# Kernel optimization log

Hardware: AMD Instinct MI355X
Metric: run time of the kernel (lower is better)

Reference implementation:

```python
import jax, jax.numpy as jnp
import numpy as np

B, T, C = 4, 2048, 2048
H = 16
D = C // H  # head_dim = 128


def setup_inputs() -> dict:
    key = jax.random.key(0)
    ks = jax.random.split(key, 11)
    s = 0.02
    return {
        "q": jax.random.normal(ks[0], (B, T, C), jnp.float32),
        "k": jax.random.normal(ks[1], (B, T, C), jnp.float32),
        "v": jax.random.normal(ks[2], (B, T, C), jnp.float32),
        "Wq": jax.random.normal(ks[3], (C, C), jnp.float32) * s,
        "bq": jnp.zeros((C,), jnp.float32),
        "Wk": jax.random.normal(ks[4], (C, C), jnp.float32) * s,
        "bk": jnp.zeros((C,), jnp.float32),
        "Wv": jax.random.normal(ks[5], (C, C), jnp.float32) * s,
        "bv": jnp.zeros((C,), jnp.float32),
        "Wo": jax.random.normal(ks[6], (C, C), jnp.float32) * s,
        "bo": jnp.zeros((C,), jnp.float32),
    }


def reference(q, k, v, Wq, bq, Wk, bk, Wv, bv, Wo, bo):
    # torch Linear: y = x @ W.T + b
    def heads(x, W, b):
        y = x @ W.T + b                      # [B,T,C]
        return y.reshape(B, T, H, D).transpose(0, 2, 1, 3)  # [B,H,T,D]

    q_h = heads(q, Wq, bq)
    k_h = heads(k, Wk, bk)
    v_h = heads(v, Wv, bv)

    scale = D ** -0.5
    scores = jnp.einsum('bhqd,bhkd->bhqk', q_h, k_h) * scale  # [B,H,T,T]
    # causal mask (is_causal=True)
    causal = jnp.tril(jnp.ones((T, T), dtype=bool))
    scores = jnp.where(causal, scores, -jnp.inf)
    probs = jax.nn.softmax(scores, axis=-1)
    out = jnp.einsum('bhqk,bhkd->bhqd', probs, v_h)           # [B,H,T,D]
    out = out.transpose(0, 2, 1, 3).reshape(B, T, C)
    return out @ Wo.T + bo
```

## Files before the change

kernel.cpp:

```cpp
#include <hip/hip_runtime.h>
#include <hip/hip_bf16.h>
#include <cmath>


#define DEV __device__ __forceinline__

typedef short short8 __attribute__((ext_vector_type(8)));
typedef float floatx4 __attribute__((ext_vector_type(4)));

#define LDS16(gp, lp)                                                        \
  __builtin_amdgcn_global_load_lds(                                          \
      (const __attribute__((address_space(1))) void*)(gp),                   \
      (__attribute__((address_space(3))) void*)(lp), 16, 0, 0)

DEV unsigned short f2bf(float f) {
  unsigned u = __builtin_bit_cast(unsigned, f);
  u += 0x7fffu + ((u >> 16) & 1u);
  return (unsigned short)(u >> 16);
}

DEV floatx4 mfma16(short8 a, short8 b, floatx4 c) {
  return __builtin_amdgcn_mfma_f32_16x16x32_bf16(a, b, c, 0, 0, 0);
}

struct Cvt7Args {
  const float* in[7];
  unsigned short* out[7];
  int n4[7];
};

__global__ __launch_bounds__(256) void cvt7_kernel(Cvt7Args a) {
  const int s = blockIdx.y;
  const float* __restrict__ in = a.in[s];
  unsigned short* __restrict__ out = a.out[s];
  const int n4 = a.n4[s];
  int stride = gridDim.x * blockDim.x;
  for (int i = blockIdx.x * blockDim.x + threadIdx.x; i < n4; i += stride) {
    float4 v = reinterpret_cast<const float4*>(in)[i];
    ushort4 o;
    o.x = f2bf(v.x); o.y = f2bf(v.y); o.z = f2bf(v.z); o.w = f2bf(v.w);
    reinterpret_cast<ushort4*>(out)[i] = o;
  }
}

DEV void gemm256_core(const unsigned short* __restrict__ aT,
                      const unsigned short* __restrict__ bT,
                      unsigned short* lds, const int K, floatx4 (&acc)[8][4]) {
  const int t = threadIdx.x;
  const int l = t & 63;
  const int w = t >> 6;
  const int wm = w >> 2, wn = w & 3;
  const int lr = l & 15, lg = l >> 4;
  const int NT = K >> 5;

  const int rA0 = t >> 2;
  const int chA0 = (t & 3) ^ ((rA0 >> 1) & 3);
  const int rA1 = (t + 512) >> 2;
  const int chA1 = (t & 3) ^ ((rA1 >> 1) & 3);

  auto stage = [&](int kt, int buf) {
    unsigned short* dst = lds + buf * 16384;
    const unsigned short* ga = aT + kt * 32;
    const unsigned short* gb = bT + kt * 32;
    LDS16(ga + (size_t)rA0 * K + chA0 * 8, dst + t * 8);
    LDS16(ga + (size_t)rA1 * K + chA1 * 8, dst + (t + 512) * 8);
    LDS16(gb + (size_t)rA0 * K + chA0 * 8, dst + 8192 + t * 8);
    LDS16(gb + (size_t)rA1 * K + chA1 * 8, dst + 8192 + (t + 512) * 8);
  };

  stage(0, 0);
  stage(1, 1);
  stage(2, 2);
  asm volatile("s_waitcnt vmcnt(8)" ::: "memory");
  __builtin_amdgcn_s_barrier();
  asm volatile("" ::: "memory");

  for (int tt = 0; tt < NT; ++tt) {
    const unsigned short* lA = lds + (tt & 3) * 16384;
    const unsigned short* lB = lA + 8192;
    if (tt + 3 < NT) stage(tt + 3, (tt + 3) & 3);
    short8 aF[8], bF[4];
#pragma unroll
    for (int ni = 0; ni < 4; ni++) {
      int row = wn * 64 + ni * 16 + lr;
      bF[ni] = *(const short8*)&lB[row * 32 + ((lg ^ ((row >> 1) & 3)) * 8)];
    }
#pragma unroll
    for (int mi = 0; mi < 8; mi++) {
      int row = wm * 128 + mi * 16 + lr;
      aF[mi] = *(const short8*)&lA[row * 32 + ((lg ^ ((row >> 1) & 3)) * 8)];
    }
    __builtin_amdgcn_s_setprio(1);
#pragma unroll
    for (int mi = 0; mi < 8; mi++)
#pragma unroll
      for (int ni = 0; ni < 4; ni++)
        acc[mi][ni] = mfma16(aF[mi], bF[ni], acc[mi][ni]);
    __builtin_amdgcn_s_setprio(0);
    if (tt + 1 < NT) {
      if (tt + 4 <= NT)
        asm volatile("s_waitcnt vmcnt(8)" ::: "memory");
      else if (tt + 3 == NT)
        asm volatile("s_waitcnt vmcnt(4)" ::: "memory");
      else
        asm volatile("s_waitcnt vmcnt(0)" ::: "memory");
      __builtin_amdgcn_s_barrier();
      asm volatile("" ::: "memory");
    }
  }
}

__global__ __launch_bounds__(512, 2) void gemm256_proj3(
    const unsigned short* __restrict__ qb, const unsigned short* __restrict__ kb,
    const unsigned short* __restrict__ vb, const unsigned short* __restrict__ wqb,
    const unsigned short* __restrict__ wkb, const unsigned short* __restrict__ wvb,
    const float* __restrict__ bq, const float* __restrict__ bk,
    const float* __restrict__ bv, unsigned short* __restrict__ Qp,
    unsigned short* __restrict__ Kp, unsigned short* __restrict__ Vt,
    float qscale) {
  constexpr int K = 2048, N = 2048;
  __shared__ unsigned short lds[65536];
  const int seg = blockIdx.x >> 8;
  int inner = blockIdx.x & 255;
  inner = (inner & 7) * 32 + (inner >> 3);
  const int bm = inner >> 3, bn = inner & 7;

  const unsigned short* A = (seg == 0) ? qb : (seg == 1) ? kb : vb;
  const unsigned short* Bw = (seg == 0) ? wqb : (seg == 1) ? wkb : wvb;
  const float* bias = (seg == 0) ? bq : (seg == 1) ? bk : bv;

  floatx4 zero = {0.f, 0.f, 0.f, 0.f};
  floatx4 acc[8][4];
#pragma unroll
  for (int i = 0; i < 8; i++)
#pragma unroll
    for (int j = 0; j < 4; j++) acc[i][j] = zero;

  gemm256_core(A + (size_t)bm * 256 * K, Bw + (size_t)bn * 256 * K, lds, K, acc);

  const int t = threadIdx.x, l = t & 63, w = t >> 6;
  const int wm = w >> 2, wn = w & 3;
  const int lr = l & 15, lg = l >> 4;
  const float oscale = (seg == 0) ? qscale : 1.0f;
#pragma unroll
  for (int ni = 0; ni < 4; ni++) {
    int gc = bn * 256 + wn * 64 + ni * 16 + lr;
    float bvv = bias[gc];
#pragma unroll
    for (int mi = 0; mi < 8; mi++) {
      int gr0 = bm * 256 + wm * 128 + mi * 16 + lg * 4;
      if (seg == 2) {
        int b = gr0 >> 11, tt0 = gr0 & 2047, h = gc >> 7, d = gc & 127;
        ushort4 v4;
        v4.x = f2bf(acc[mi][ni][0] + bvv);
        v4.y = f2bf(acc[mi][ni][1] + bvv);
        v4.z = f2bf(acc[mi][ni][2] + bvv);
        v4.w = f2bf(acc[mi][ni][3] + bvv);
        *(ushort4*)&Vt[((size_t)(b * 16 + h) << 18) + (d << 11) + tt0] = v4;
      } else {
        unsigned short* dst = (seg == 0) ? Qp : Kp;
#pragma unroll
        for (int r = 0; r < 4; r++)
          dst[(size_t)(gr0 + r) * N + gc] =
              f2bf((acc[mi][ni][r] + bvv) * oscale);
      }
    }
  }
}

__global__ __launch_bounds__(512, 2) void gemm256_out(
    const unsigned short* __restrict__ A, const unsigned short* __restrict__ Bw,
    const float* __restrict__ bias, float* __restrict__ outp) {
  constexpr int K = 2048, N = 2048;
  __shared__ unsigned short lds[65536];
  int inner = blockIdx.x;
  inner = (inner & 7) * 32 + (inner >> 3);
  const int bm = inner >> 3, bn = inner & 7;

  floatx4 zero = {0.f, 0.f, 0.f, 0.f};
  floatx4 acc[8][4];
#pragma unroll
  for (int i = 0; i < 8; i++)
#pragma unroll
    for (int j = 0; j < 4; j++) acc[i][j] = zero;

  gemm256_core(A + (size_t)bm * 256 * K, Bw + (size_t)bn * 256 * K, lds, K, acc);

  const int t = threadIdx.x, l = t & 63, w = t >> 6;
  const int wm = w >> 2, wn = w & 3;
  const int lr = l & 15, lg = l >> 4;
#pragma unroll
  for (int ni = 0; ni < 4; ni++) {
    int gc = bn * 256 + wn * 64 + ni * 16 + lr;
    float bvv = bias[gc];
#pragma unroll
    for (int mi = 0; mi < 8; mi++) {
      int gr0 = bm * 256 + wm * 128 + mi * 16 + lg * 4;
#pragma unroll
      for (int r = 0; r < 4; r++)
        outp[(size_t)(gr0 + r) * N + gc] = acc[mi][ni][r] + bvv;
    }
  }
}

__global__ __launch_bounds__(512, 2) void attn_kernel(
    const unsigned short* __restrict__ Qp, const unsigned short* __restrict__ Kp,
    const unsigned short* __restrict__ Vt, unsigned short* __restrict__ Out) {
  constexpr int T = 2048, C = 2048;
  __shared__ unsigned short lds[49152];
  unsigned short* sP = lds + 32768;

  const int bid = blockIdx.x;
  const int swz = (bid & 7) * 32 + (bid >> 3);
  const int bh = swz >> 2;
  const int pr = swz & 3;
  const int b = bh >> 4, h = bh & 15;
  const int t = threadIdx.x, l = t & 63, w = t >> 6;
  const int lr = l & 15, lg = l >> 4, l7 = l & 7;

  const unsigned short* Kg = Kp + (size_t)(b * T) * C + h * 128;
  const unsigned short* Vg = Vt + ((size_t)bh << 18);

  auto stage_kv = [&](int kb, int buf) {
    unsigned short* dK = lds + (buf ? 8192 : 0);
    unsigned short* dV = lds + 16384 + (buf ? 8192 : 0);
#pragma unroll
    for (int i = 0; i < 2; i++) {
      int c = t + i * 512;
      int row = c >> 4, cc = c & 15;
      LDS16(Kg + (size_t)(kb + row) * C + (cc ^ (row & 7)) * 8, &dK[c * 8]);
    }
#pragma unroll
    for (int i = 0; i < 2; i++) {
      int c = t + i * 512;
      int d = c >> 3, cc = c & 7;
      LDS16(Vg + (size_t)d * T + kb + (cc ^ (d & 7)) * 8, &dV[c * 8]);
    }
  };

  for (int seg = 0; seg < 2; seg++) {
    const int qs = seg ? pr : 7 - pr;
    const unsigned short* Qg = Qp + (size_t)(b * T + qs * 256) * C + h * 128;

#pragma unroll
    for (int i = 0; i < 8; i++) {
      int c = t + i * 512;
      int row = c >> 4, cc = c & 15;
      LDS16(Qg + (size_t)row * C + cc * 8, &lds[c * 8]);
    }
    __syncthreads();
    const int qw = qs * 256 + w * 32;
    short8 qf[2][4];
#pragma unroll
    for (int mi = 0; mi < 2; mi++)
#pragma unroll
      for (int ks = 0; ks < 4; ks++)
        qf[mi][ks] = *(const short8*)&lds[(w * 32 + mi * 16 + lr) * 128 +
                                          ks * 32 + lg * 8];
    __syncthreads();

    floatx4 zero = {0.f, 0.f, 0.f, 0.f};
    floatx4 oacc[2][8];
#pragma unroll
    for (int i = 0; i < 2; i++)
#pragma unroll
      for (int j = 0; j < 8; j++) oacc[i][j] = zero;
    float mold[2][4], lsum[2][4];
#pragma unroll
    for (int i = 0; i < 2; i++)
#pragma unroll
      for (int r = 0; r < 4; r++) { mold[i][r] = -1e30f; lsum[i][r] = 0.f; }

    const int ntile = 4 * qs + 4;
    stage_kv(0, 0);
    __syncthreads();
    int cur = 0;
    for (int tile = 0; tile < ntile; tile++) {
      const int kbase = tile * 64;
      if (tile + 1 < ntile) stage_kv(kbase + 64, cur ^ 1);
      const unsigned short* sK = lds + (cur ? 8192 : 0);
      const unsigned short* sV = lds + 16384 + (cur ? 8192 : 0);
      if (kbase <= qw + 31) {
        floatx4 sc[2][4];
#pragma unroll
        for (int i = 0; i < 2; i++)
#pragma unroll
          for (int j = 0; j < 4; j++) sc[i][j] = zero;
        __builtin_amdgcn_s_setprio(1);
#pragma unroll
        for (int ks = 0; ks < 4; ks++) {
#pragma unroll
          for (int ni = 0; ni < 4; ni++) {
            int R = ni * 16 + lr;
            short8 bF = *(const short8*)&sK[R * 128 + ((ks * 4 + lg) ^ l7) * 8];
#pragma unroll
            for (int mi = 0; mi < 2; mi++)
              sc[mi][ni] = mfma16(qf[mi][ks], bF, sc[mi][ni]);
          }
        }
        __builtin_amdgcn_s_setprio(0);
        if (kbase + 63 > qw) {
#pragma unroll
          for (int mi = 0; mi < 2; mi++)
#pragma unroll
            for (int ni = 0; ni < 4; ni++)
#pragma unroll
              for (int r = 0; r < 4; r++) {
                int col = kbase + ni * 16 + lr;
                int row = qw + mi * 16 + lg * 4 + r;
                if (col > row) sc[mi][ni][r] = -1e30f;
              }
        }
#pragma unroll
        for (int mi = 0; mi < 2; mi++) {
          float xr[4];
          int dok = 1;
#pragma unroll
          for (int r = 0; r < 4; r++) {
            float x = fmaxf(fmaxf(sc[mi][0][r], sc[mi][1][r]),
                            fmaxf(sc[mi][2][r], sc[mi][3][r]));
            x = fmaxf(x, __shfl_xor(x, 1));
            x = fmaxf(x, __shfl_xor(x, 2));
            x = fmaxf(x, __shfl_xor(x, 4));
            x = fmaxf(x, __shfl_xor(x, 8));
            xr[r] = x;
            dok &= (x - mold[mi][r] <= 8.0f) ? 1 : 0;
          }
          const bool defer = __all(dok);
          float al[4];
          if (!defer) {
#pragma unroll
            for (int r = 0; r < 4; r++) {
              float m2 = fmaxf(mold[mi][r], xr[r]);
              al[r] = __builtin_amdgcn_exp2f(mold[mi][r] - m2);
              mold[mi][r] = m2;
            }
          }
          float rs[4] = {0.f, 0.f, 0.f, 0.f};
#pragma unroll
          for (int ni = 0; ni < 4; ni++)
#pragma unroll
            for (int r = 0; r < 4; r++) {
              float p = __builtin_amdgcn_exp2f(sc[mi][ni][r] - mold[mi][r]);
              sc[mi][ni][r] = p;
              rs[r] += p;
            }
#pragma unroll
          for (int r = 0; r < 4; r++) {
            float s = rs[r];
            s += __shfl_xor(s, 1);
            s += __shfl_xor(s, 2);
            s += __shfl_xor(s, 4);
            s += __shfl_xor(s, 8);
            rs[r] = s;
          }
          if (!defer) {
#pragma unroll
            for (int r = 0; r < 4; r++)
              lsum[mi][r] = lsum[mi][r] * al[r] + rs[r];
#pragma unroll
            for (int ni = 0; ni < 8; ni++)
#pragma unroll
              for (int r = 0; r < 4; r++) oacc[mi][ni][r] *= al[r];
          } else {
#pragma unroll
            for (int r = 0; r < 4; r++) lsum[mi][r] += rs[r];
          }
#pragma unroll
          for (int ni = 0; ni < 4; ni++)
#pragma unroll
            for (int r = 0; r < 4; r++) {
              int rr = mi * 16 + lg * 4 + r;
              int ch = (ni * 2 + ((l >> 3) & 1)) ^ (rr & 7);
              sP[w * 2048 + rr * 64 + ch * 8 + l7] = f2bf(sc[mi][ni][r]);
            }
        }
        __builtin_amdgcn_s_setprio(1);
#pragma unroll
        for (int ks = 0; ks < 2; ks++) {
          short8 pf[2];
#pragma unroll
          for (int mi = 0; mi < 2; mi++)
            pf[mi] = *(const short8*)&sP[w * 2048 + (mi * 16 + lr) * 64 +
                                         ((ks * 4 + lg) ^ l7) * 8];
#pragma unroll
          for (int ni = 0; ni < 8; ni++) {
            int d = ni * 16 + lr;
            short8 vF = *(const short8*)&sV[d * 64 + ((ks * 4 + lg) ^ l7) * 8];
#pragma unroll
            for (int mi = 0; mi < 2; mi++)
              oacc[mi][ni] = mfma16(pf[mi], vF, oacc[mi][ni]);
          }
        }
        __builtin_amdgcn_s_setprio(0);
      }
      __syncthreads();
      cur ^= 1;
    }
    unsigned short* Og = Out + (size_t)(b * T + qw) * C + h * 128;
#pragma unroll
    for (int mi = 0; mi < 2; mi++) {
      float rl[4];
#pragma unroll
      for (int r = 0; r < 4; r++) rl[r] = 1.0f / lsum[mi][r];
#pragma unroll
      for (int ni = 0; ni < 8; ni++)
#pragma unroll
        for (int r = 0; r < 4; r++)
          Og[(size_t)(mi * 16 + lg * 4 + r) * C + ni * 16 + lr] =
              f2bf(oacc[mi][ni][r] * rl[r]);
    }
    __syncthreads();
  }
}

extern "C" void kernel_launch(void* const* d_in, const int* in_sizes, int n_in,
                              void* d_out, int out_size, void* d_ws,
                              size_t ws_size, hipStream_t stream) {
  const float* q = (const float*)d_in[0];
  const float* k = (const float*)d_in[1];
  const float* v = (const float*)d_in[2];
  const float* Wq = (const float*)d_in[3];
  const float* bq = (const float*)d_in[4];
  const float* Wk = (const float*)d_in[5];
  const float* bk = (const float*)d_in[6];
  const float* Wv = (const float*)d_in[7];
  const float* bv = (const float*)d_in[8];
  const float* Wo = (const float*)d_in[9];
  const float* bo = (const float*)d_in[10];

  const int B = 4, T = 2048, C = 2048;
  const size_t E = (size_t)B * T * C;
  const size_t WE = (size_t)C * C;
  unsigned short* ws = (unsigned short*)d_ws;
  unsigned short* qb = ws;
  unsigned short* kb = ws + E;
  unsigned short* vb = ws + 2 * E;
  unsigned short* wqb = ws + 3 * E;
  unsigned short* wkb = wqb + WE;
  unsigned short* wvb = wqb + 2 * WE;
  unsigned short* wob = wqb + 3 * WE;
  unsigned short* Qp = ws + 4 * E;
  unsigned short* Kp = ws + 5 * E;
  unsigned short* Vtb = ws + 6 * E;
  unsigned short* attn = qb;

  Cvt7Args ca;
  ca.in[0] = q;  ca.out[0] = qb;  ca.n4[0] = (int)(E / 4);
  ca.in[1] = k;  ca.out[1] = kb;  ca.n4[1] = (int)(E / 4);
  ca.in[2] = v;  ca.out[2] = vb;  ca.n4[2] = (int)(E / 4);
  ca.in[3] = Wq; ca.out[3] = wqb; ca.n4[3] = (int)(WE / 4);
  ca.in[4] = Wk; ca.out[4] = wkb; ca.n4[4] = (int)(WE / 4);
  ca.in[5] = Wv; ca.out[5] = wvb; ca.n4[5] = (int)(WE / 4);
  ca.in[6] = Wo; ca.out[6] = wob; ca.n4[6] = (int)(WE / 4);
  cvt7_kernel<<<dim3(512, 7), 256, 0, stream>>>(ca);

  const float qscale = 1.4426950408889634f / sqrtf(128.0f);
  gemm256_proj3<<<768, 512, 0, stream>>>(qb, kb, vb, wqb, wkb, wvb, bq, bk, bv,
                                         Qp, Kp, Vtb, qscale);

  attn_kernel<<<256, 512, 0, stream>>>(Qp, Kp, Vtb, attn);

  gemm256_out<<<256, 512, 0, stream>>>(attn, wob, bo, (float*)d_out);
}
```

Measured before the change: 531.7 us.

## Double KV tile to 128 keys and stream P through a small per-warp buffer

Raises the attention key tile from 64 to 128 rows, so each tile needs fewer barriers and fewer softmax rescale steps, and the K/V staging buffers double in size. The probability matrix is no longer written for the whole tile at once. Each warp writes P for a 32-key chunk into a small swizzled buffer and immediately consumes it in the PV MFMAs. LDS grows from 96KB to 144KB and the score registers double, which may cut the occupancy of two blocks per CU allowed by the launch bounds and raise register pressure.

```diff
diff --git a/kernel.cpp b/kernel.cpp
--- a/kernel.cpp
+++ b/kernel.cpp
@@ -207,8 +207,7 @@
     const unsigned short* __restrict__ Qp, const unsigned short* __restrict__ Kp,
     const unsigned short* __restrict__ Vt, unsigned short* __restrict__ Out) {
   constexpr int T = 2048, C = 2048;
-  __shared__ unsigned short lds[49152];
-  unsigned short* sP = lds + 32768;
+  __shared__ unsigned short lds[73728];
 
   const int bid = blockIdx.x;
   const int swz = (bid & 7) * 32 + (bid >> 3);
@@ -217,23 +216,24 @@
   const int b = bh >> 4, h = bh & 15;
   const int t = threadIdx.x, l = t & 63, w = t >> 6;
   const int lr = l & 15, lg = l >> 4, l7 = l & 7;
+  unsigned short* sPw = lds + 65536 + w * 1024;
 
   const unsigned short* Kg = Kp + (size_t)(b * T) * C + h * 128;
   const unsigned short* Vg = Vt + ((size_t)bh << 18);
 
   auto stage_kv = [&](int kb, int buf) {
-    unsigned short* dK = lds + (buf ? 8192 : 0);
-    unsigned short* dV = lds + 16384 + (buf ? 8192 : 0);
-#pragma unroll
-    for (int i = 0; i < 2; i++) {
+    unsigned short* dK = lds + buf * 16384;
+    unsigned short* dV = lds + 32768 + buf * 16384;
+#pragma unroll
+    for (int i = 0; i < 4; i++) {
       int c = t + i * 512;
       int row = c >> 4, cc = c & 15;
       LDS16(Kg + (size_t)(kb + row) * C + (cc ^ (row & 7)) * 8, &dK[c * 8]);
     }
 #pragma unroll
-    for (int i = 0; i < 2; i++) {
+    for (int i = 0; i < 4; i++) {
       int c = t + i * 512;
-      int d = c >> 3, cc = c & 7;
+      int d = c >> 4, cc = c & 15;
       LDS16(Vg + (size_t)d * T + kb + (cc ^ (d & 7)) * 8, &dV[c * 8]);
     }
   };
@@ -271,26 +271,26 @@
 #pragma unroll
       for (int r = 0; r < 4; r++) { mold[i][r] = -1e30f; lsum[i][r] = 0.f; }
 
-    const int ntile = 4 * qs + 4;
+    const int ntile = 2 * qs + 2;
     stage_kv(0, 0);
     __syncthreads();
     int cur = 0;
     for (int tile = 0; tile < ntile; tile++) {
-      const int kbase = tile * 64;
-      if (tile + 1 < ntile) stage_kv(kbase + 64, cur ^ 1);
-      const unsigned short* sK = lds + (cur ? 8192 : 0);
-      const unsigned short* sV = lds + 16384 + (cur ? 8192 : 0);
+      const int kbase = tile * 128;
+      if (tile + 1 < ntile) stage_kv(kbase + 128, cur ^ 1);
+      const unsigned short* sK = lds + cur * 16384;
+      const unsigned short* sV = lds + 32768 + cur * 16384;
       if (kbase <= qw + 31) {
-        floatx4 sc[2][4];
+        floatx4 sc[2][8];
 #pragma unroll
         for (int i = 0; i < 2; i++)
 #pragma unroll
-          for (int j = 0; j < 4; j++) sc[i][j] = zero;
+          for (int j = 0; j < 8; j++) sc[i][j] = zero;
         __builtin_amdgcn_s_setprio(1);
 #pragma unroll
         for (int ks = 0; ks < 4; ks++) {
 #pragma unroll
-          for (int ni = 0; ni < 4; ni++) {
+          for (int ni = 0; ni < 8; ni++) {
             int R = ni * 16 + lr;
             short8 bF = *(const short8*)&sK[R * 128 + ((ks * 4 + lg) ^ l7) * 8];
 #pragma unroll
@@ -299,11 +299,11 @@
           }
         }
         __builtin_amdgcn_s_setprio(0);
-        if (kbase + 63 > qw) {
+        if (kbase + 127 > qw) {
 #pragma unroll
           for (int mi = 0; mi < 2; mi++)
 #pragma unroll
-            for (int ni = 0; ni < 4; ni++)
+            for (int ni = 0; ni < 8; ni++)
 #pragma unroll
               for (int r = 0; r < 4; r++) {
                 int col = kbase + ni * 16 + lr;
@@ -317,8 +317,10 @@
           int dok = 1;
 #pragma unroll
           for (int r = 0; r < 4; r++) {
-            float x = fmaxf(fmaxf(sc[mi][0][r], sc[mi][1][r]),
-                            fmaxf(sc[mi][2][r], sc[mi][3][r]));
+            float x = fmaxf(fmaxf(fmaxf(sc[mi][0][r], sc[mi][1][r]),
+                                  fmaxf(sc[mi][2][r], sc[mi][3][r])),
+                            fmaxf(fmaxf(sc[mi][4][r], sc[mi][5][r]),
+                                  fmaxf(sc[mi][6][r], sc[mi][7][r])));
             x = fmaxf(x, __shfl_xor(x, 1));
             x = fmaxf(x, __shfl_xor(x, 2));
             x = fmaxf(x, __shfl_xor(x, 4));
@@ -338,7 +340,7 @@
           }
           float rs[4] = {0.f, 0.f, 0.f, 0.f};
 #pragma unroll
-          for (int ni = 0; ni < 4; ni++)
+          for (int ni = 0; ni < 8; ni++)
 #pragma unroll
             for (int r = 0; r < 4; r++) {
               float p = __builtin_amdgcn_exp2f(sc[mi][ni][r] - mold[mi][r]);
@@ -366,27 +368,33 @@
 #pragma unroll
             for (int r = 0; r < 4; r++) lsum[mi][r] += rs[r];
           }
-#pragma unroll
-          for (int ni = 0; ni < 4; ni++)
-#pragma unroll
-            for (int r = 0; r < 4; r++) {
-              int rr = mi * 16 + lg * 4 + r;
-              int ch = (ni * 2 + ((l >> 3) & 1)) ^ (rr & 7);
-              sP[w * 2048 + rr * 64 + ch * 8 + l7] = f2bf(sc[mi][ni][r]);
-            }
         }
         __builtin_amdgcn_s_setprio(1);
 #pragma unroll
-        for (int ks = 0; ks < 2; ks++) {
+        for (int p = 0; p < 4; p++) {
+#pragma unroll
+          for (int mi = 0; mi < 2; mi++)
+#pragma unroll
+            for (int dn = 0; dn < 2; dn++)
+#pragma unroll
+              for (int r = 0; r < 4; r++) {
+                int ni = p * 2 + dn;
+                int rr = mi * 16 + lg * 4 + r;
+                int lch = (dn * 2 + (lr >> 3)) ^ ((rr >> 1) & 3);
+                sPw[rr * 32 + lch * 8 + l7] = f2bf(sc[mi][ni][r]);
+              }
           short8 pf[2];
 #pragma unroll
-          for (int mi = 0; mi < 2; mi++)
-            pf[mi] = *(const short8*)&sP[w * 2048 + (mi * 16 + lr) * 64 +
-                                         ((ks * 4 + lg) ^ l7) * 8];
+          for (int mi = 0; mi < 2; mi++) {
+            int rr2 = mi * 16 + lr;
+            pf[mi] =
+                *(const short8*)&sPw[rr2 * 32 + ((lg ^ ((rr2 >> 1) & 3)) * 8)];
+          }
 #pragma unroll
           for (int ni = 0; ni < 8; ni++) {
             int d = ni * 16 + lr;
-            short8 vF = *(const short8*)&sV[d * 64 + ((ks * 4 + lg) ^ l7) * 8];
+            short8 vF =
+                *(const short8*)&sV[d * 128 + (((p * 4 + lg) ^ l7) * 8)];
 #pragma unroll
             for (int mi = 0; mi < 2; mi++)
               oacc[mi][ni] = mfma16(pf[mi], vF, oacc[mi][ni]);
```

Result: slower. 558.6 us (+5.1%).

## Make QKV projection persistent over three segments with cross-segment prefetch

Applied to the files above, without the earlier changes.

The QKV projection kernel now launches one block per output tile (256 blocks) and loops over the Q, K and V GEMMs inside each block. It uses a 4-deep LDS pipeline and prefetches the first three K-tiles of the next segment while the current epilogue runs, which hides the pipeline fill between GEMMs and the wave-launch tail. It also drops a trailing __syncthreads in the attention kernel. The risk is reduced parallelism: 256 blocks at 2 per CU may leave CUs underused. The longer per-block work may also hurt load balance.

```diff
diff --git a/kernel.cpp b/kernel.cpp
--- a/kernel.cpp
+++ b/kernel.cpp
@@ -119,50 +119,128 @@
     unsigned short* __restrict__ Kp, unsigned short* __restrict__ Vt,
     float qscale) {
   constexpr int K = 2048, N = 2048;
+  constexpr int NT = K >> 5;
   __shared__ unsigned short lds[65536];
-  const int seg = blockIdx.x >> 8;
-  int inner = blockIdx.x & 255;
+  int inner = blockIdx.x;
   inner = (inner & 7) * 32 + (inner >> 3);
   const int bm = inner >> 3, bn = inner & 7;
-
-  const unsigned short* A = (seg == 0) ? qb : (seg == 1) ? kb : vb;
-  const unsigned short* Bw = (seg == 0) ? wqb : (seg == 1) ? wkb : wvb;
-  const float* bias = (seg == 0) ? bq : (seg == 1) ? bk : bv;
-
-  floatx4 zero = {0.f, 0.f, 0.f, 0.f};
-  floatx4 acc[8][4];
-#pragma unroll
-  for (int i = 0; i < 8; i++)
-#pragma unroll
-    for (int j = 0; j < 4; j++) acc[i][j] = zero;
-
-  gemm256_core(A + (size_t)bm * 256 * K, Bw + (size_t)bn * 256 * K, lds, K, acc);
 
   const int t = threadIdx.x, l = t & 63, w = t >> 6;
   const int wm = w >> 2, wn = w & 3;
   const int lr = l & 15, lg = l >> 4;
-  const float oscale = (seg == 0) ? qscale : 1.0f;
-#pragma unroll
-  for (int ni = 0; ni < 4; ni++) {
-    int gc = bn * 256 + wn * 64 + ni * 16 + lr;
-    float bvv = bias[gc];
-#pragma unroll
-    for (int mi = 0; mi < 8; mi++) {
-      int gr0 = bm * 256 + wm * 128 + mi * 16 + lg * 4;
-      if (seg == 2) {
-        int b = gr0 >> 11, tt0 = gr0 & 2047, h = gc >> 7, d = gc & 127;
-        ushort4 v4;
-        v4.x = f2bf(acc[mi][ni][0] + bvv);
-        v4.y = f2bf(acc[mi][ni][1] + bvv);
-        v4.z = f2bf(acc[mi][ni][2] + bvv);
-        v4.w = f2bf(acc[mi][ni][3] + bvv);
-        *(ushort4*)&Vt[((size_t)(b * 16 + h) << 18) + (d << 11) + tt0] = v4;
-      } else {
-        unsigned short* dst = (seg == 0) ? Qp : Kp;
-#pragma unroll
-        for (int r = 0; r < 4; r++)
-          dst[(size_t)(gr0 + r) * N + gc] =
-              f2bf((acc[mi][ni][r] + bvv) * oscale);
+  const int rA0 = t >> 2;
+  const int chA0 = (t & 3) ^ ((rA0 >> 1) & 3);
+  const int rA1 = (t + 512) >> 2;
+  const int chA1 = (t & 3) ^ ((rA1 >> 1) & 3);
+
+  auto stage = [&](const unsigned short* aT, const unsigned short* bT, int kt,
+                   int buf) {
+    unsigned short* dst = lds + buf * 16384;
+    const unsigned short* ga = aT + kt * 32;
+    const unsigned short* gb = bT + kt * 32;
+    LDS16(ga + (size_t)rA0 * K + chA0 * 8, dst + t * 8);
+    LDS16(ga + (size_t)rA1 * K + chA1 * 8, dst + (t + 512) * 8);
+    LDS16(gb + (size_t)rA0 * K + chA0 * 8, dst + 8192 + t * 8);
+    LDS16(gb + (size_t)rA1 * K + chA1 * 8, dst + 8192 + (t + 512) * 8);
+  };
+
+  {
+    const unsigned short* aT = qb + (size_t)bm * 256 * K;
+    const unsigned short* bT = wqb + (size_t)bn * 256 * K;
+    stage(aT, bT, 0, 0);
+    stage(aT, bT, 1, 1);
+    stage(aT, bT, 2, 2);
+  }
+
+  for (int seg = 0; seg < 3; ++seg) {
+    const unsigned short* A = (seg == 0) ? qb : (seg == 1) ? kb : vb;
+    const unsigned short* Bw = (seg == 0) ? wqb : (seg == 1) ? wkb : wvb;
+    const float* bias = (seg == 0) ? bq : (seg == 1) ? bk : bv;
+    const unsigned short* aT = A + (size_t)bm * 256 * K;
+    const unsigned short* bT = Bw + (size_t)bn * 256 * K;
+
+    if (seg == 0)
+      asm volatile("s_waitcnt vmcnt(8)" ::: "memory");
+    else
+      asm volatile("s_waitcnt vmcnt(0)" ::: "memory");
+    __builtin_amdgcn_s_barrier();
+    asm volatile("" ::: "memory");
+
+    floatx4 zero = {0.f, 0.f, 0.f, 0.f};
+    floatx4 acc[8][4];
+#pragma unroll
+    for (int i = 0; i < 8; i++)
+#pragma unroll
+      for (int j = 0; j < 4; j++) acc[i][j] = zero;
+
+    for (int tt = 0; tt < NT; ++tt) {
+      const unsigned short* lA = lds + (tt & 3) * 16384;
+      const unsigned short* lB = lA + 8192;
+      if (tt + 3 < NT) stage(aT, bT, tt + 3, (tt + 3) & 3);
+      short8 aF[8], bF[4];
+#pragma unroll
+      for (int ni = 0; ni < 4; ni++) {
+        int row = wn * 64 + ni * 16 + lr;
+        bF[ni] = *(const short8*)&lB[row * 32 + ((lg ^ ((row >> 1) & 3)) * 8)];
+      }
+#pragma unroll
+      for (int mi = 0; mi < 8; mi++) {
+        int row = wm * 128 + mi * 16 + lr;
+        aF[mi] = *(const short8*)&lA[row * 32 + ((lg ^ ((row >> 1) & 3)) * 8)];
+      }
+      __builtin_amdgcn_s_setprio(1);
+#pragma unroll
+      for (int mi = 0; mi < 8; mi++)
+#pragma unroll
+        for (int ni = 0; ni < 4; ni++)
+          acc[mi][ni] = mfma16(aF[mi], bF[ni], acc[mi][ni]);
+      __builtin_amdgcn_s_setprio(0);
+      if (tt + 1 < NT) {
+        if (tt + 4 <= NT)
+          asm volatile("s_waitcnt vmcnt(8)" ::: "memory");
+        else if (tt + 3 == NT)
+          asm volatile("s_waitcnt vmcnt(4)" ::: "memory");
+        else
+          asm volatile("s_waitcnt vmcnt(0)" ::: "memory");
+        __builtin_amdgcn_s_barrier();
+        asm volatile("" ::: "memory");
+      }
+    }
+    __syncthreads();
+
+    if (seg < 2) {
+      const unsigned short* A2 = (seg == 0) ? kb : vb;
+      const unsigned short* B2 = (seg == 0) ? wkb : wvb;
+      const unsigned short* aT2 = A2 + (size_t)bm * 256 * K;
+      const unsigned short* bT2 = B2 + (size_t)bn * 256 * K;
+      stage(aT2, bT2, 0, 0);
+      stage(aT2, bT2, 1, 1);
+      stage(aT2, bT2, 2, 2);
+    }
+
+    const float oscale = (seg == 0) ? qscale : 1.0f;
+#pragma unroll
+    for (int ni = 0; ni < 4; ni++) {
+      int gc = bn * 256 + wn * 64 + ni * 16 + lr;
+      float bvv = bias[gc];
+#pragma unroll
+      for (int mi = 0; mi < 8; mi++) {
+        int gr0 = bm * 256 + wm * 128 + mi * 16 + lg * 4;
+        if (seg == 2) {
+          int b = gr0 >> 11, tt0 = gr0 & 2047, h = gc >> 7, d = gc & 127;
+          ushort4 v4;
+          v4.x = f2bf(acc[mi][ni][0] + bvv);
+          v4.y = f2bf(acc[mi][ni][1] + bvv);
+          v4.z = f2bf(acc[mi][ni][2] + bvv);
+          v4.w = f2bf(acc[mi][ni][3] + bvv);
+          *(ushort4*)&Vt[((size_t)(b * 16 + h) << 18) + (d << 11) + tt0] = v4;
+        } else {
+          unsigned short* dst = (seg == 0) ? Qp : Kp;
+#pragma unroll
+          for (int r = 0; r < 4; r++)
+            dst[(size_t)(gr0 + r) * N + gc] =
+                f2bf((acc[mi][ni][r] + bvv) * oscale);
+        }
       }
     }
   }
@@ -410,7 +488,6 @@
           Og[(size_t)(mi * 16 + lg * 4 + r) * C + ni * 16 + lr] =
               f2bf(oacc[mi][ni][r] * rl[r]);
     }
-    __syncthreads();
   }
 }
 
@@ -456,7 +533,7 @@
   cvt7_kernel<<<dim3(512, 7), 256, 0, stream>>>(ca);
 
   const float qscale = 1.4426950408889634f / sqrtf(128.0f);
-  gemm256_proj3<<<768, 512, 0, stream>>>(qb, kb, vb, wqb, wkb, wvb, bq, bk, bv,
+  gemm256_proj3<<<256, 512, 0, stream>>>(qb, kb, vb, wqb, wkb, wvb, bq, bk, bv,
                                          Qp, Kp, Vtb, qscale);
 
   attn_kernel<<<256, 512, 0, stream>>>(Qp, Kp, Vtb, attn);
```

Measured after the change: 554.9 us. 1.04x slower.
